# Performance work log

Hardware: AMD Instinct MI355X
Metric: run time of the kernel (lower is better)

Reference implementation:

```python
import jax, jax.numpy as jnp
import numpy as np


def setup_inputs() -> dict:
    key = jax.random.key(0)
    ks = jax.random.split(key, 12)
    B, T, n, m = 128, 64, 81, 128
    inp = {
        "X": jax.random.normal(ks[0], (B, T, n), dtype=jnp.float32),
        "h0": jax.random.normal(ks[1], (B, m), dtype=jnp.float32),
        "s0": jax.random.normal(ks[2], (B, m), dtype=jnp.float32),
        "W_lstm": jax.random.normal(ks[3], (n, 4 * m), dtype=jnp.float32) * 0.05,
        "U_lstm": jax.random.normal(ks[4], (m, 4 * m), dtype=jnp.float32) * 0.05,
        "b_lstm": jax.random.normal(ks[5], (4 * m,), dtype=jnp.float32) * 0.05,
        "We_w": jax.random.normal(ks[6], (2 * m, T), dtype=jnp.float32) * 0.05,
        "We_b": jax.random.normal(ks[7], (T,), dtype=jnp.float32) * 0.05,
        "Ue_w": jax.random.normal(ks[8], (T, T), dtype=jnp.float32) * 0.05,
        "Ue_b": jax.random.normal(ks[9], (T,), dtype=jnp.float32) * 0.05,
        "ve_w": jax.random.normal(ks[10], (T, 1), dtype=jnp.float32) * 0.05,
        "ve_b": jax.random.normal(ks[11], (1,), dtype=jnp.float32) * 0.05,
    }
    return inp


def reference(X, h0, s0, W_lstm, U_lstm, b_lstm, We_w, We_b, Ue_w, Ue_b, ve_w, ve_b):
    # Faithful to the TF code: initial_state=[h0, s0] is re-passed at every t,
    # so each timestep is an INDEPENDENT single LSTM cell step from (h0, s0).
    # This lets us vectorize the whole Python loop over t.
    B, T, n = X.shape
    m = h0.shape[1]
    # gates for all timesteps at once: (B, T, 4m). Keras gate order: i, f, g(c), o.
    gates = jnp.einsum('btn,ng->btg', X, W_lstm) + (h0 @ U_lstm + b_lstm)[:, None, :]
    i = jax.nn.sigmoid(gates[..., 0 * m:1 * m])
    f = jax.nn.sigmoid(gates[..., 1 * m:2 * m])
    g = jnp.tanh(gates[..., 2 * m:3 * m])
    o = jax.nn.sigmoid(gates[..., 3 * m:4 * m])
    c = f * s0[:, None, :] + i * g          # (B, T, m)
    h = o * jnp.tanh(c)                     # (B, T, m)
    # Input attention, vectorized over t.
    hc = jnp.concatenate([h, c], axis=-1)   # (B, T, 2m)
    A = hc @ We_w + We_b                    # (B, T, T)  = W_e([h;c]) per step t
    U = jnp.einsum('btn,tk->bnk', X, Ue_w) + Ue_b  # (B, n, T) = U_e(X^T)
    # e[b,t,i] = v_e(tanh(A[b,t,:] + U[b,i,:]))
    e = jnp.tanh(A[:, :, None, :] + U[:, None, :, :])       # (B, T, n, T)
    scores = jnp.einsum('btnk,k->btn', e, ve_w[:, 0]) + ve_b[0]  # (B, T, n)
    alpha = jax.nn.softmax(scores, axis=-1)                 # (B, T, n)
    # stack() gives (T, B, 1, n); tf.multiply broadcasts with X (B, T, n) -> (T, B, T, n)
    out = X[None, :, :, :] * jnp.transpose(alpha, (1, 0, 2))[:, :, None, :]
    return out
```

## Files before the change

kernel.cpp:

```cpp
#include <hip/hip_runtime.h>
#include <math.h>

#define BB 128
#define TT_ 64
#define NN 81
#define MM 128
#define GG 512
#define TN 5184
#define TCH 8
#define NBLK2 (BB * (TT_ / TCH))
#define SC_ 2.8853900817779268f

__device__ __forceinline__ float sigmoidf_(float x) {
    return 1.0f / (1.0f + __expf(-x));
}
__device__ __forceinline__ float fast_tanh(float x) {
    float e = __expf(2.0f * x);
    return 1.0f - 2.0f / (e + 1.0f);
}

__global__ __launch_bounds__(256) void k1_prep(
    const float* __restrict__ X, const float* __restrict__ h0,
    const float* __restrict__ U_lstm, const float* __restrict__ b_lstm,
    const float* __restrict__ Ue_w, const float* __restrict__ Ue_b,
    float* __restrict__ ws_hb, float* __restrict__ ws_U)
{
    __shared__ float Xl[TN];
    __shared__ float sUe[64 * 16];
    __shared__ float h0l[MM];

    int blk = blockIdx.x;
    int b = blk >> 2;
    int q = blk & 3;
    int tid = threadIdx.x;

    for (int p = tid; p < TN; p += 256) Xl[p] = X[b * TN + p];
    for (int p = tid; p < 1024; p += 256) {
        int t = p >> 4, kl = p & 15;
        sUe[p] = Ue_w[t * TT_ + q * 16 + kl];
    }
    if (q == 0 && tid < MM) h0l[tid] = h0[b * MM + tid];
    __syncthreads();

    if (q == 0) {
        float2 bl = ((const float2*)b_lstm)[tid];
        float a0 = bl.x, a1 = bl.y;
        for (int j = 0; j < MM; ++j) {
            float h = h0l[j];
            float2 w = ((const float2*)&U_lstm[j * GG])[tid];
            a0 += h * w.x;
            a1 += h * w.y;
        }
        ((float2*)&ws_hb[b * GG])[tid] = make_float2(a0, a1);
    }

    int kl = tid & 15;
    int k  = q * 16 + kl;
    int ir = tid >> 4;
    float ueb = Ue_b[k];
#pragma unroll
    for (int pass = 0; pass < 6; ++pass) {
        int i = pass * 16 + ir;
        if (i < NN) {
            float acc = ueb;
#pragma unroll 8
            for (int t = 0; t < TT_; ++t)
                acc += Xl[t * NN + i] * sUe[t * 16 + kl];
            ws_U[b * TN + i * 64 + k] = acc;
        }
    }
}

__global__ __launch_bounds__(256) void k2_main(
    const float* __restrict__ X, const float* __restrict__ s0,
    const float* __restrict__ W_lstm,
    const float* __restrict__ We_w, const float* __restrict__ We_b,
    const float* __restrict__ ve_w, const float* __restrict__ ve_b,
    const float* __restrict__ ws_hb, const float* __restrict__ ws_U,
    float* __restrict__ out)
{
    __shared__ alignas(16) float sXct[NN * TCH];
    __shared__ float sGU[5280];
    __shared__ float sHc[TCH * 256];
    __shared__ float sA[TCH * 65];
    __shared__ float sSc[TCH * NN];
    __shared__ float sVe[TT_];

    int blk = blockIdx.x;
    int b  = blk >> 3;
    int tc = blk & 7;
    int t0 = tc * TCH;
    int tid = threadIdx.x;
    float veb = ve_b[0];

    for (int p = tid; p < NN * TCH; p += 256) {
        float v = X[b * TN + t0 * NN + p];
        int tt = p / NN, np = p - tt * NN;
        sXct[np * TCH + tt] = v;
    }
    if (tid < TT_) sVe[tid] = ve_w[tid];
    __syncthreads();

    float acc0[TCH], acc1[TCH];
    {
        float2 hbv = ((const float2*)&ws_hb[b * GG])[tid];
#pragma unroll
        for (int tt = 0; tt < TCH; ++tt) { acc0[tt] = hbv.x; acc1[tt] = hbv.y; }
        for (int n = 0; n < NN; ++n) {
            float2 w = ((const float2*)&W_lstm[n * GG])[tid];
            const float4* xr4 = (const float4*)&sXct[n * TCH];
            float4 xa = xr4[0];
            float4 xb = xr4[1];
            acc0[0] += xa.x * w.x; acc1[0] += xa.x * w.y;
            acc0[1] += xa.y * w.x; acc1[1] += xa.y * w.y;
            acc0[2] += xa.z * w.x; acc1[2] += xa.z * w.y;
            acc0[3] += xa.w * w.x; acc1[3] += xa.w * w.y;
            acc0[4] += xb.x * w.x; acc1[4] += xb.x * w.y;
            acc0[5] += xb.y * w.x; acc1[5] += xb.y * w.y;
            acc0[6] += xb.z * w.x; acc1[6] += xb.z * w.y;
            acc0[7] += xb.w * w.x; acc1[7] += xb.w * w.y;
        }
    }
#pragma unroll
    for (int tt = 0; tt < TCH; ++tt) {
        ((float2*)&sGU[tt * GG])[tid] = make_float2(acc0[tt], acc1[tt]);
    }
    __syncthreads();

    for (int p = tid; p < TCH * MM; p += 256) {
        int tt = p >> 7, u = p & 127;
        const float* gr = &sGU[tt * GG];
        float gi = sigmoidf_(gr[u]);
        float gf = sigmoidf_(gr[MM + u]);
        float gg = fast_tanh(gr[2 * MM + u]);
        float go = sigmoidf_(gr[3 * MM + u]);
        float c  = gf * s0[b * MM + u] + gi * gg;
        float h  = go * fast_tanh(c);
        sHc[tt * 256 + u]       = h;
        sHc[tt * 256 + 128 + u] = c;
    }
    __syncthreads();

    {
        int k  = tid & 63;
        int th = tid >> 6;
        float a0 = We_b[k], a1 = a0;
        for (int j = 0; j < 256; ++j) {
            float w = We_w[j * TT_ + k];
            a0 += sHc[th * 256 + j]       * w;
            a1 += sHc[(th + 4) * 256 + j] * w;
        }
        sA[th * 65 + k]       = a0 * SC_;
        sA[(th + 4) * 65 + k] = a1 * SC_;
    }
    for (int p = tid; p < TN; p += 256) {
        int i = p >> 6, k = p & 63;
        sGU[i * 65 + k] = ws_U[b * TN + p] * SC_;
    }
    __syncthreads();

    {
        int wv = tid >> 6;
        int l  = tid & 63;
        float sumVe = 0.f;
        for (int k = 0; k < TT_; ++k) sumVe += sVe[k];
#pragma unroll
        for (int hh = 0; hh < 2; ++hh) {
            int tt = wv + hh * 4;
            const float* Ar = &sA[tt * 65];
#pragma unroll
            for (int pass = 0; pass < 2; ++pass) {
                int i = l + pass * 64;
                if (i < NN) {
                    const float* Ur = &sGU[i * 65];
                    float acc = 0.f;
#pragma unroll 8
                    for (int k = 0; k < TT_; ++k) {
                        float s = Ar[k] + Ur[k];
                        float e = exp2f(s);
                        float r = __builtin_amdgcn_rcpf(e + 1.0f);
                        acc = fmaf(sVe[k], r, acc);
                    }
                    sSc[tt * NN + i] = sumVe - 2.0f * acc + veb;
                }
            }
        }
    }
    __syncthreads();

    {
        int wv = tid >> 6;
        int l  = tid & 63;
#pragma unroll
        for (int hh = 0; hh < 2; ++hh) {
            int tt = wv + hh * 4;
            float a  = sSc[tt * NN + l];
            bool v2  = (l + 64 < NN);
            float b2 = v2 ? sSc[tt * NN + l + 64] : -1e30f;
            float mx = fmaxf(a, b2);
            for (int d = 32; d >= 1; d >>= 1) mx = fmaxf(mx, __shfl_xor(mx, d, 64));
            float ea = __expf(a - mx);
            float eb = v2 ? __expf(b2 - mx) : 0.f;
            float s = ea + eb;
            for (int d = 32; d >= 1; d >>= 1) s += __shfl_xor(s, d, 64);
            float inv = 1.f / s;
            sSc[tt * NN + l] = ea * inv;
            if (v2) sSc[tt * NN + l + 64] = eb * inv;
        }
    }
    __syncthreads();

    {
        const float* Xb = &X[b * TN];
        for (int j = tid; j < TN; j += 256) {
            float x = Xb[j];
            int i = j % NN;
#pragma unroll
            for (int tt = 0; tt < TCH; ++tt) {
                out[((size_t)(t0 + tt) * BB + b) * TN + j] = x * sSc[tt * NN + i];
            }
        }
    }
}

extern "C" void kernel_launch(void* const* d_in, const int* in_sizes, int n_in,
                              void* d_out, int out_size, void* d_ws, size_t ws_size,
                              hipStream_t stream) {
    const float* X      = (const float*)d_in[0];
    const float* h0     = (const float*)d_in[1];
    const float* s0     = (const float*)d_in[2];
    const float* W_lstm = (const float*)d_in[3];
    const float* U_lstm = (const float*)d_in[4];
    const float* b_lstm = (const float*)d_in[5];
    const float* We_w   = (const float*)d_in[6];
    const float* We_b   = (const float*)d_in[7];
    const float* Ue_w   = (const float*)d_in[8];
    const float* Ue_b   = (const float*)d_in[9];
    const float* ve_w   = (const float*)d_in[10];
    const float* ve_b   = (const float*)d_in[11];
    float* out = (float*)d_out;

    float* ws    = (float*)d_ws;
    float* ws_hb = ws;
    float* ws_U  = ws + BB * GG;

    k1_prep<<<BB * 4, 256, 0, stream>>>(X, h0, U_lstm, b_lstm, Ue_w, Ue_b, ws_hb, ws_U);
    k2_main<<<NBLK2, 256, 0, stream>>>(X, s0, W_lstm, We_w, We_b, ve_w, ve_b,
                                       ws_hb, ws_U, out);
}
```

Baseline: 250.4 us.

## Fuse LSTM gate activation into GEMM registers and merge scores with softmax

Each thread now accumulates all four gates for one hidden unit across four timesteps, so gate activations and cell updates are applied straight from registers. This removes the shared-memory gate buffer and one barrier. The attention-score loop is merged with the softmax in registers, dropping another barrier and the score round-trip, and the U tile is loaded together with X at kernel start. The SC_ scale on U moves into the prep kernel and launch bounds request 4 blocks per CU, which may constrain registers and cause spills.

```diff
diff --git a/kernel.cpp b/kernel.cpp
--- a/kernel.cpp
+++ b/kernel.cpp
@@ -66,12 +66,12 @@
 #pragma unroll 8
             for (int t = 0; t < TT_; ++t)
                 acc += Xl[t * NN + i] * sUe[t * 16 + kl];
-            ws_U[b * TN + i * 64 + k] = acc;
-        }
-    }
-}
-
-__global__ __launch_bounds__(256) void k2_main(
+            ws_U[b * TN + i * 64 + k] = acc * SC_;
+        }
+    }
+}
+
+__global__ __launch_bounds__(256, 4) void k2_main(
     const float* __restrict__ X, const float* __restrict__ s0,
     const float* __restrict__ W_lstm,
     const float* __restrict__ We_w, const float* __restrict__ We_b,
@@ -80,7 +80,7 @@
     float* __restrict__ out)
 {
     __shared__ alignas(16) float sXct[NN * TCH];
-    __shared__ float sGU[5280];
+    __shared__ float sU[NN * 65];
     __shared__ float sHc[TCH * 256];
     __shared__ float sA[TCH * 65];
     __shared__ float sSc[TCH * NN];
@@ -91,122 +91,123 @@
     int tc = blk & 7;
     int t0 = tc * TCH;
     int tid = threadIdx.x;
+    int u    = tid & 127;
+    int half = tid >> 7;
     float veb = ve_b[0];
+
+    float hb0 = ws_hb[b * GG + u];
+    float hb1 = ws_hb[b * GG + 128 + u];
+    float hb2 = ws_hb[b * GG + 256 + u];
+    float hb3 = ws_hb[b * GG + 384 + u];
+    float s0v = s0[b * MM + u];
 
     for (int p = tid; p < NN * TCH; p += 256) {
         float v = X[b * TN + t0 * NN + p];
         int tt = p / NN, np = p - tt * NN;
         sXct[np * TCH + tt] = v;
     }
+    for (int p = tid; p < TN; p += 256) {
+        int i = p >> 6, k = p & 63;
+        sU[i * 65 + k] = ws_U[b * TN + p];
+    }
     if (tid < TT_) sVe[tid] = ve_w[tid];
     __syncthreads();
 
-    float acc0[TCH], acc1[TCH];
-    {
-        float2 hbv = ((const float2*)&ws_hb[b * GG])[tid];
-#pragma unroll
-        for (int tt = 0; tt < TCH; ++tt) { acc0[tt] = hbv.x; acc1[tt] = hbv.y; }
+    float acc[4][4];
+#pragma unroll
+    for (int r = 0; r < 4; ++r) {
+        acc[r][0] = hb0; acc[r][1] = hb1; acc[r][2] = hb2; acc[r][3] = hb3;
+    }
+    {
+        const float* Wl = &W_lstm[u];
         for (int n = 0; n < NN; ++n) {
-            float2 w = ((const float2*)&W_lstm[n * GG])[tid];
-            const float4* xr4 = (const float4*)&sXct[n * TCH];
-            float4 xa = xr4[0];
-            float4 xb = xr4[1];
-            acc0[0] += xa.x * w.x; acc1[0] += xa.x * w.y;
-            acc0[1] += xa.y * w.x; acc1[1] += xa.y * w.y;
-            acc0[2] += xa.z * w.x; acc1[2] += xa.z * w.y;
-            acc0[3] += xa.w * w.x; acc1[3] += xa.w * w.y;
-            acc0[4] += xb.x * w.x; acc1[4] += xb.x * w.y;
-            acc0[5] += xb.y * w.x; acc1[5] += xb.y * w.y;
-            acc0[6] += xb.z * w.x; acc1[6] += xb.z * w.y;
-            acc0[7] += xb.w * w.x; acc1[7] += xb.w * w.y;
-        }
-    }
-#pragma unroll
-    for (int tt = 0; tt < TCH; ++tt) {
-        ((float2*)&sGU[tt * GG])[tid] = make_float2(acc0[tt], acc1[tt]);
-    }
-    __syncthreads();
-
-    for (int p = tid; p < TCH * MM; p += 256) {
-        int tt = p >> 7, u = p & 127;
-        const float* gr = &sGU[tt * GG];
-        float gi = sigmoidf_(gr[u]);
-        float gf = sigmoidf_(gr[MM + u]);
-        float gg = fast_tanh(gr[2 * MM + u]);
-        float go = sigmoidf_(gr[3 * MM + u]);
-        float c  = gf * s0[b * MM + u] + gi * gg;
+            float w0 = Wl[n * GG];
+            float w1 = Wl[n * GG + 128];
+            float w2 = Wl[n * GG + 256];
+            float w3 = Wl[n * GG + 384];
+            float4 xv = *(const float4*)&sXct[n * TCH + 4 * half];
+            acc[0][0] += xv.x * w0; acc[0][1] += xv.x * w1; acc[0][2] += xv.x * w2; acc[0][3] += xv.x * w3;
+            acc[1][0] += xv.y * w0; acc[1][1] += xv.y * w1; acc[1][2] += xv.y * w2; acc[1][3] += xv.y * w3;
+            acc[2][0] += xv.z * w0; acc[2][1] += xv.z * w1; acc[2][2] += xv.z * w2; acc[2][3] += xv.z * w3;
+            acc[3][0] += xv.w * w0; acc[3][1] += xv.w * w1; acc[3][2] += xv.w * w2; acc[3][3] += xv.w * w3;
+        }
+    }
+#pragma unroll
+    for (int r = 0; r < 4; ++r) {
+        int tt = 4 * half + r;
+        float gi = sigmoidf_(acc[r][0]);
+        float gf = sigmoidf_(acc[r][1]);
+        float gg = fast_tanh(acc[r][2]);
+        float go = sigmoidf_(acc[r][3]);
+        float c  = gf * s0v + gi * gg;
         float h  = go * fast_tanh(c);
         sHc[tt * 256 + u]       = h;
         sHc[tt * 256 + 128 + u] = c;
     }
     __syncthreads();
 
-    {
-        int k  = tid & 63;
-        int th = tid >> 6;
-        float a0 = We_b[k], a1 = a0;
+    int wv = tid >> 6;
+    int l  = tid & 63;
+
+    {
+        float a0 = We_b[l], a1 = a0;
+        const float* Wep = &We_w[l];
         for (int j = 0; j < 256; ++j) {
-            float w = We_w[j * TT_ + k];
-            a0 += sHc[th * 256 + j]       * w;
-            a1 += sHc[(th + 4) * 256 + j] * w;
-        }
-        sA[th * 65 + k]       = a0 * SC_;
-        sA[(th + 4) * 65 + k] = a1 * SC_;
-    }
-    for (int p = tid; p < TN; p += 256) {
-        int i = p >> 6, k = p & 63;
-        sGU[i * 65 + k] = ws_U[b * TN + p] * SC_;
-    }
-    __syncthreads();
-
-    {
-        int wv = tid >> 6;
-        int l  = tid & 63;
-        float sumVe = 0.f;
-        for (int k = 0; k < TT_; ++k) sumVe += sVe[k];
-#pragma unroll
-        for (int hh = 0; hh < 2; ++hh) {
-            int tt = wv + hh * 4;
-            const float* Ar = &sA[tt * 65];
-#pragma unroll
-            for (int pass = 0; pass < 2; ++pass) {
-                int i = l + pass * 64;
-                if (i < NN) {
-                    const float* Ur = &sGU[i * 65];
-                    float acc = 0.f;
+            float w  = Wep[j * TT_];
+            a0 += sHc[wv * 256 + j]       * w;
+            a1 += sHc[(wv + 4) * 256 + j] * w;
+        }
+        sA[wv * 65 + l]       = a0 * SC_;
+        sA[(wv + 4) * 65 + l] = a1 * SC_;
+    }
+    float sumVe;
+    {
+        float sv = sVe[l];
+        sumVe = sv;
+        for (int d = 32; d >= 1; d >>= 1) sumVe += __shfl_xor(sumVe, d, 64);
+    }
+
+#pragma unroll
+    for (int hh = 0; hh < 2; ++hh) {
+        int tt = wv + hh * 4;
+        const float* Ar = &sA[tt * 65];
+        float sc0, sc1;
+        {
+            const float* Ur = &sU[l * 65];
+            float a2 = 0.f;
 #pragma unroll 8
-                    for (int k = 0; k < TT_; ++k) {
-                        float s = Ar[k] + Ur[k];
-                        float e = exp2f(s);
-                        float r = __builtin_amdgcn_rcpf(e + 1.0f);
-                        acc = fmaf(sVe[k], r, acc);
-                    }
-                    sSc[tt * NN + i] = sumVe - 2.0f * acc + veb;
-                }
+            for (int k = 0; k < TT_; ++k) {
+                float s = Ar[k] + Ur[k];
+                float e = exp2f(s);
+                float r2 = __builtin_amdgcn_rcpf(e + 1.0f);
+                a2 = fmaf(sVe[k], r2, a2);
             }
-        }
-    }
-    __syncthreads();
-
-    {
-        int wv = tid >> 6;
-        int l  = tid & 63;
-#pragma unroll
-        for (int hh = 0; hh < 2; ++hh) {
-            int tt = wv + hh * 4;
-            float a  = sSc[tt * NN + l];
-            bool v2  = (l + 64 < NN);
-            float b2 = v2 ? sSc[tt * NN + l + 64] : -1e30f;
-            float mx = fmaxf(a, b2);
-            for (int d = 32; d >= 1; d >>= 1) mx = fmaxf(mx, __shfl_xor(mx, d, 64));
-            float ea = __expf(a - mx);
-            float eb = v2 ? __expf(b2 - mx) : 0.f;
-            float s = ea + eb;
-            for (int d = 32; d >= 1; d >>= 1) s += __shfl_xor(s, d, 64);
-            float inv = 1.f / s;
-            sSc[tt * NN + l] = ea * inv;
-            if (v2) sSc[tt * NN + l + 64] = eb * inv;
-        }
+            sc0 = sumVe - 2.0f * a2 + veb;
+        }
+        bool v2 = (l + 64 < NN);
+        if (v2) {
+            const float* Ur = &sU[(l + 64) * 65];
+            float a2 = 0.f;
+#pragma unroll 8
+            for (int k = 0; k < TT_; ++k) {
+                float s = Ar[k] + Ur[k];
+                float e = exp2f(s);
+                float r2 = __builtin_amdgcn_rcpf(e + 1.0f);
+                a2 = fmaf(sVe[k], r2, a2);
+            }
+            sc1 = sumVe - 2.0f * a2 + veb;
+        } else {
+            sc1 = -1e30f;
+        }
+        float mx = fmaxf(sc0, sc1);
+        for (int d = 32; d >= 1; d >>= 1) mx = fmaxf(mx, __shfl_xor(mx, d, 64));
+        float ea = __expf(sc0 - mx);
+        float eb = v2 ? __expf(sc1 - mx) : 0.f;
+        float s = ea + eb;
+        for (int d = 32; d >= 1; d >>= 1) s += __shfl_xor(s, d, 64);
+        float inv = 1.f / s;
+        sSc[tt * NN + l] = ea * inv;
+        if (v2) sSc[tt * NN + l + 64] = eb * inv;
     }
     __syncthreads();
 
```

Result: no change. 250.0 us (-0.2%).
